# Optimization experiments

Measured on AMD Instinct MI355X. Metric: run time of the kernel, lower is better.

Reference implementation:

```python
import jax, jax.numpy as jnp
import numpy as np

N_NODES = 100000
D_FEAT = 128
BATCH = 32768
K_NEIGH = 32
NUM_SAMPLE = 10


def setup_inputs() -> dict:
    key = jax.random.key(0)
    k1, k2, k3 = jax.random.split(key, 3)
    features = jax.random.normal(k1, (N_NODES, D_FEAT), dtype=jnp.float32)
    nodes = jax.random.randint(k2, (BATCH,), 0, N_NODES)
    neighs = jax.random.randint(k3, (BATCH, K_NEIGH), 0, N_NODES)
    return {"features": features, "nodes": nodes, "neighs": neighs, "num_sample": NUM_SAMPLE}


def reference(features, nodes, neighs, num_sample):
    # Gather center and candidate-neighbor features from the node table.
    center = features[nodes]            # [B, D]
    neigh_feats = features[neighs]      # [B, K, D]
    # Cosine similarity of each center to each of its K candidate neighbors
    # (matches similarity = center @ neighbors^T / (||center|| * ||neighbors||)).
    dots = jnp.einsum('bd,bkd->bk', center, neigh_feats)                 # [B, K]
    c_norm = jnp.linalg.norm(center, axis=-1, keepdims=True)             # [B, 1]
    n_norm = jnp.linalg.norm(neigh_feats, axis=-1)                       # [B, K]
    sim = dots / (c_norm * n_norm)
    # Top-num_sample neighbor selection by descending similarity
    # (replaces the per-node torch.sort + list slicing).
    _, top_idx = jax.lax.top_k(sim, num_sample)                          # [B, k]
    # Masked mean over selected neighbors (replaces the dense mask.mm(embed_matrix))
    sel = jnp.take_along_axis(neigh_feats, top_idx[..., None], axis=1)   # [B, k, D]
    to_feats = jax.nn.relu(jnp.mean(sel, axis=1))                        # [B, D]
    return to_feats
```

## Files before the change

kernel.cpp:

```cpp
#include <hip/hip_runtime.h>

#define K_NEIGH 32
#define D_FEAT  128

__device__ __forceinline__ float readlane_f(float v, int l) {
    return __int_as_float(__builtin_amdgcn_readlane(__float_as_int(v), l));
}

__global__ __launch_bounds__(256, 3) void intra_agg_kernel(
    const float* __restrict__ features,
    const int*   __restrict__ nodes,
    const int*   __restrict__ neighs,
    const int*   __restrict__ num_sample_p,
    float*       __restrict__ out,
    int batch)
{
    const int tid  = blockIdx.x * blockDim.x + threadIdx.x;
    const int lane = threadIdx.x & 63;
    int b = tid >> 6;
    if (b >= batch) return;
    b = __builtin_amdgcn_readfirstlane(b);

    const int  ns = *num_sample_p;
    const int* nb = neighs + (size_t)b * K_NEIGH;

    const int   cnode = nodes[b];
    const float2 c2 = ((const float2*)(features + (size_t)cnode * D_FEAT))[lane];

    float2 rows[K_NEIGH];
    #pragma unroll
    for (int r = 0; r < K_NEIGH; ++r) {
        const int nidx = nb[r];
        rows[r] = ((const float2*)(features + (size_t)nidx * D_FEAT))[lane];
    }

    float cc = c2.x * c2.x + c2.y * c2.y;
    #pragma unroll
    for (int m = 32; m >= 1; m >>= 1) cc += __shfl_xor(cc, m);
    const float cn = sqrtf(cc);

    float dt[K_NEIGH], n2[K_NEIGH];
    #pragma unroll
    for (int r = 0; r < K_NEIGH; ++r) {
        dt[r] = c2.x * rows[r].x + c2.y * rows[r].y;
        n2[r] = rows[r].x * rows[r].x + rows[r].y * rows[r].y;
    }

    #pragma unroll
    for (int o = 32; o >= 2; o >>= 1) {
        const bool up = (lane & o) != 0;
        #pragma unroll
        for (int r = 0; r < o / 2; ++r) {
            const float sd = up ? dt[r] : dt[r + o / 2];
            const float sn = up ? n2[r] : n2[r + o / 2];
            const float rd = __shfl_xor(sd, o);
            const float rn = __shfl_xor(sn, o);
            const float kd = up ? dt[r + o / 2] : dt[r];
            const float kn = up ? n2[r + o / 2] : n2[r];
            dt[r] = kd + rd;
            n2[r] = kn + rn;
        }
    }
    dt[0] += __shfl_xor(dt[0], 1);
    n2[0] += __shfl_xor(n2[0], 1);

    const int   myrow = lane >> 1;
    const float sim   = dt[0] / (cn * sqrtf(n2[0]));

    int rank = 0;
    #pragma unroll
    for (int j = 0; j < K_NEIGH; ++j) {
        const float sj = readlane_f(sim, 2 * j);
        rank += (sj > sim || (sj == sim && j < myrow)) ? 1 : 0;
    }

    const unsigned long long bal = __ballot(rank < ns);
    unsigned long long x = bal & 0x5555555555555555ull;
    x = (x | (x >> 1))  & 0x3333333333333333ull;
    x = (x | (x >> 2))  & 0x0F0F0F0F0F0F0F0Full;
    x = (x | (x >> 4))  & 0x00FF00FF00FF00FFull;
    x = (x | (x >> 8))  & 0x0000FFFF0000FFFFull;
    x = (x | (x >> 16)) & 0x00000000FFFFFFFFull;
    const unsigned mask = (unsigned)x;

    float2 acc = make_float2(0.f, 0.f);
    #pragma unroll
    for (int r = 0; r < K_NEIGH; ++r) {
        const float s = (float)((mask >> r) & 1u);
        acc.x = fmaf(rows[r].x, s, acc.x);
        acc.y = fmaf(rows[r].y, s, acc.y);
    }
    const float nsf = (float)ns;
    float2 ov;
    ov.x = fmaxf(acc.x / nsf, 0.f);
    ov.y = fmaxf(acc.y / nsf, 0.f);
    ((float2*)(out + (size_t)b * D_FEAT))[lane] = ov;
}

extern "C" void kernel_launch(void* const* d_in, const int* in_sizes, int n_in,
                              void* d_out, int out_size, void* d_ws, size_t ws_size,
                              hipStream_t stream) {
    const float* features = (const float*)d_in[0];
    const int*   nodes    = (const int*)d_in[1];
    const int*   neighs   = (const int*)d_in[2];
    const int*   ns       = (const int*)d_in[3];
    float*       out      = (float*)d_out;

    const int batch  = in_sizes[1];
    const int blocks = (batch + 3) / 4;

    intra_agg_kernel<<<blocks, 256, 0, stream>>>(features, nodes, neighs, ns, out, batch);
}
```

Baseline: 153.4 us.

## Stage neighbor rows as bf16 in LDS and accumulate only selected rows

New measurement: 305.7 us. 1.99x slower.

```diff
diff --git a/kernel.cpp b/kernel.cpp
--- a/kernel.cpp
+++ b/kernel.cpp
@@ -1,13 +1,16 @@
 #include <hip/hip_runtime.h>
+#include <hip/hip_bf16.h>
 
 #define K_NEIGH 32
 #define D_FEAT  128
+#define WPB     4
+#define RSTRIDE 65
 
 __device__ __forceinline__ float readlane_f(float v, int l) {
     return __int_as_float(__builtin_amdgcn_readlane(__float_as_int(v), l));
 }
 
-__global__ __launch_bounds__(256, 3) void intra_agg_kernel(
+__global__ __launch_bounds__(256, 4) void intra_agg_kernel(
     const float* __restrict__ features,
     const int*   __restrict__ nodes,
     const int*   __restrict__ neighs,
@@ -15,8 +18,11 @@
     float*       __restrict__ out,
     int batch)
 {
+    __shared__ unsigned s_rows[WPB][K_NEIGH * RSTRIDE];
+
     const int tid  = blockIdx.x * blockDim.x + threadIdx.x;
     const int lane = threadIdx.x & 63;
+    const int w    = threadIdx.x >> 6;
     int b = tid >> 6;
     if (b >= batch) return;
     b = __builtin_amdgcn_readfirstlane(b);
@@ -24,16 +30,8 @@
     const int  ns = *num_sample_p;
     const int* nb = neighs + (size_t)b * K_NEIGH;
 
-    const int   cnode = nodes[b];
+    const int    cnode = nodes[b];
     const float2 c2 = ((const float2*)(features + (size_t)cnode * D_FEAT))[lane];
-
-    float2 rows[K_NEIGH];
-    #pragma unroll
-    for (int r = 0; r < K_NEIGH; ++r) {
-        const int nidx = nb[r];
-        rows[r] = ((const float2*)(features + (size_t)nidx * D_FEAT))[lane];
-    }
-
     float cc = c2.x * c2.x + c2.y * c2.y;
     #pragma unroll
     for (int m = 32; m >= 1; m >>= 1) cc += __shfl_xor(cc, m);
@@ -42,8 +40,12 @@
     float dt[K_NEIGH], n2[K_NEIGH];
     #pragma unroll
     for (int r = 0; r < K_NEIGH; ++r) {
-        dt[r] = c2.x * rows[r].x + c2.y * rows[r].y;
-        n2[r] = rows[r].x * rows[r].x + rows[r].y * rows[r].y;
+        const int    nidx = nb[r];
+        const float2 v = ((const float2*)(features + (size_t)nidx * D_FEAT))[lane];
+        dt[r] = c2.x * v.x + c2.y * v.y;
+        n2[r] = v.x * v.x + v.y * v.y;
+        const __hip_bfloat162 h = __float22bfloat162_rn(v);
+        s_rows[w][r * RSTRIDE + lane] = *(const unsigned*)&h;
     }
 
     #pragma unroll
@@ -81,14 +83,16 @@
     x = (x | (x >> 4))  & 0x00FF00FF00FF00FFull;
     x = (x | (x >> 8))  & 0x0000FFFF0000FFFFull;
     x = (x | (x >> 16)) & 0x00000000FFFFFFFFull;
-    const unsigned mask = (unsigned)x;
+    unsigned mask = (unsigned)x;
+    mask = __builtin_amdgcn_readfirstlane(mask);
 
     float2 acc = make_float2(0.f, 0.f);
-    #pragma unroll
-    for (int r = 0; r < K_NEIGH; ++r) {
-        const float s = (float)((mask >> r) & 1u);
-        acc.x = fmaf(rows[r].x, s, acc.x);
-        acc.y = fmaf(rows[r].y, s, acc.y);
+    while (mask) {
+        const int r = __ffs(mask) - 1;
+        mask &= mask - 1;
+        const unsigned u = s_rows[w][r * RSTRIDE + lane];
+        acc.x += __uint_as_float(u << 16);
+        acc.y += __uint_as_float(u & 0xffff0000u);
     }
     const float nsf = (float)ns;
     float2 ov;
@@ -107,7 +111,7 @@
     float*       out      = (float*)d_out;
 
     const int batch  = in_sizes[1];
-    const int blocks = (batch + 3) / 4;
+    const int blocks = (batch + WPB - 1) / WPB;
 
     intra_agg_kernel<<<blocks, 256, 0, stream>>>(features, nodes, neighs, ns, out, batch);
 }
```

## Split wave into half-waves per neighbor set and re-gather selected rows

Applied to the files above, without the earlier changes.

Result: slower. 240.8 us (+56.9%).

```diff
diff --git a/kernel.cpp b/kernel.cpp
--- a/kernel.cpp
+++ b/kernel.cpp
@@ -7,7 +7,7 @@
     return __int_as_float(__builtin_amdgcn_readlane(__float_as_int(v), l));
 }
 
-__global__ __launch_bounds__(256, 3) void intra_agg_kernel(
+__global__ __launch_bounds__(256, 6) void intra_agg_kernel(
     const float* __restrict__ features,
     const int*   __restrict__ nodes,
     const int*   __restrict__ neighs,
@@ -17,6 +17,8 @@
 {
     const int tid  = blockIdx.x * blockDim.x + threadIdx.x;
     const int lane = threadIdx.x & 63;
+    const int l32  = lane & 31;
+    const int half = lane >> 5;
     int b = tid >> 6;
     if (b >= batch) return;
     b = __builtin_amdgcn_readfirstlane(b);
@@ -24,30 +26,24 @@
     const int  ns = *num_sample_p;
     const int* nb = neighs + (size_t)b * K_NEIGH;
 
-    const int   cnode = nodes[b];
-    const float2 c2 = ((const float2*)(features + (size_t)cnode * D_FEAT))[lane];
-
-    float2 rows[K_NEIGH];
+    const int    cnode = nodes[b];
+    const float4 c4 = ((const float4*)(features + (size_t)cnode * D_FEAT))[l32];
+    float cc = c4.x*c4.x + c4.y*c4.y + c4.z*c4.z + c4.w*c4.w;
     #pragma unroll
-    for (int r = 0; r < K_NEIGH; ++r) {
-        const int nidx = nb[r];
-        rows[r] = ((const float2*)(features + (size_t)nidx * D_FEAT))[lane];
-    }
-
-    float cc = c2.x * c2.x + c2.y * c2.y;
-    #pragma unroll
-    for (int m = 32; m >= 1; m >>= 1) cc += __shfl_xor(cc, m);
+    for (int m = 16; m >= 1; m >>= 1) cc += __shfl_xor(cc, m);
     const float cn = sqrtf(cc);
 
-    float dt[K_NEIGH], n2[K_NEIGH];
+    float dt[16], n2[16];
     #pragma unroll
-    for (int r = 0; r < K_NEIGH; ++r) {
-        dt[r] = c2.x * rows[r].x + c2.y * rows[r].y;
-        n2[r] = rows[r].x * rows[r].x + rows[r].y * rows[r].y;
+    for (int i = 0; i < 16; ++i) {
+        const int    nidx = nb[16 * half + i];
+        const float4 v = ((const float4*)(features + (size_t)nidx * D_FEAT))[l32];
+        dt[i] = c4.x*v.x + c4.y*v.y + c4.z*v.z + c4.w*v.w;
+        n2[i] =  v.x*v.x +  v.y*v.y +  v.z*v.z +  v.w*v.w;
     }
 
     #pragma unroll
-    for (int o = 32; o >= 2; o >>= 1) {
+    for (int o = 16; o >= 2; o >>= 1) {
         const bool up = (lane & o) != 0;
         #pragma unroll
         for (int r = 0; r < o / 2; ++r) {
@@ -64,7 +60,7 @@
     dt[0] += __shfl_xor(dt[0], 1);
     n2[0] += __shfl_xor(n2[0], 1);
 
-    const int   myrow = lane >> 1;
+    const int   myrow = (half << 4) | (l32 >> 1);
     const float sim   = dt[0] / (cn * sqrtf(n2[0]));
 
     int rank = 0;
@@ -81,20 +77,36 @@
     x = (x | (x >> 4))  & 0x00FF00FF00FF00FFull;
     x = (x | (x >> 8))  & 0x0000FFFF0000FFFFull;
     x = (x | (x >> 16)) & 0x00000000FFFFFFFFull;
-    const unsigned mask = (unsigned)x;
+    unsigned mask = __builtin_amdgcn_readfirstlane((unsigned)x);
 
-    float2 acc = make_float2(0.f, 0.f);
-    #pragma unroll
-    for (int r = 0; r < K_NEIGH; ++r) {
-        const float s = (float)((mask >> r) & 1u);
-        acc.x = fmaf(rows[r].x, s, acc.x);
-        acc.y = fmaf(rows[r].y, s, acc.y);
+    float4 acc = make_float4(0.f, 0.f, 0.f, 0.f);
+    while (mask) {
+        const int j0 = __ffs(mask) - 1; mask &= mask - 1;
+        int   j1 = 0; float w1 = 0.f;
+        if (mask) { j1 = __ffs(mask) - 1; mask &= mask - 1; w1 = 1.f; }
+        const int   j = half ? j1 : j0;
+        const float w = half ? w1 : 1.f;
+        const int nidx = nb[j];
+        const float4 r = ((const float4*)(features + (size_t)nidx * D_FEAT))[l32];
+        acc.x = fmaf(r.x, w, acc.x);
+        acc.y = fmaf(r.y, w, acc.y);
+        acc.z = fmaf(r.z, w, acc.z);
+        acc.w = fmaf(r.w, w, acc.w);
     }
-    const float nsf = (float)ns;
-    float2 ov;
-    ov.x = fmaxf(acc.x / nsf, 0.f);
-    ov.y = fmaxf(acc.y / nsf, 0.f);
-    ((float2*)(out + (size_t)b * D_FEAT))[lane] = ov;
+    acc.x += __shfl_xor(acc.x, 32);
+    acc.y += __shfl_xor(acc.y, 32);
+    acc.z += __shfl_xor(acc.z, 32);
+    acc.w += __shfl_xor(acc.w, 32);
+
+    if (half == 0) {
+        const float nsf = (float)ns;
+        float4 o;
+        o.x = fmaxf(acc.x / nsf, 0.f);
+        o.y = fmaxf(acc.y / nsf, 0.f);
+        o.z = fmaxf(acc.z / nsf, 0.f);
+        o.w = fmaxf(acc.w / nsf, 0.f);
+        ((float4*)(out + (size_t)b * D_FEAT))[l32] = o;
+    }
 }
 
 extern "C" void kernel_launch(void* const* d_in, const int* in_sizes, int n_in,
```
